# Kernel optimization log

Hardware: AMD Instinct MI355X
Metric: run time of the kernel (lower is better)

The kernel has to match this reference:

```python
import jax, jax.numpy as jnp
import numpy as np

N_NODES = 100000
N_EDGES = 1600000
C_IN = 128
C_OUT = 128


def setup_inputs() -> dict:
    key = jax.random.key(0)
    k1, k2, k3, k4, k5 = jax.random.split(key, 5)
    x = jax.random.normal(k1, (N_NODES, C_IN), dtype=jnp.float32)
    W = jax.random.normal(k2, (2 * C_IN, C_OUT), dtype=jnp.float32) * (1.0 / np.sqrt(2 * C_IN))
    b = jax.random.normal(k3, (C_OUT,), dtype=jnp.float32) * 0.01
    src = jax.random.randint(k4, (N_EDGES,), 0, N_NODES, dtype=jnp.int64 if jax.config.jax_enable_x64 else jnp.int32)
    dst = jax.random.randint(k5, (N_EDGES,), 0, N_NODES, dtype=jnp.int64 if jax.config.jax_enable_x64 else jnp.int32)
    return {"x": x, "W": W, "b": b, "src": src, "dst": dst}


def reference(x, W, b, src, dst):
    # Max-Relative graph conv: per-edge relative feature, max-aggregated per dst node.
    diff = x[dst] - x[src]                                  # [E, C]  (edge messages)
    max_diff = jax.ops.segment_max(diff, dst, num_segments=x.shape[0])  # [N, C]
    # Nodes with no incoming edges: segment_max yields -inf; zero them out.
    max_diff = jnp.where(jnp.isneginf(max_diff), jnp.zeros_like(max_diff), max_diff)
    h = jnp.concatenate([x, max_diff], axis=1)              # [N, 2C]
    return jax.nn.relu(h @ W + b)                           # Linear(2C->C_out) + ReLU
```

## Files before the change

### kernel.cpp

```cpp
#include <hip/hip_runtime.h>
#include <math.h>

#define NN 100000
#define NE 1600000
#define C 128

#define TS 4096
#define NT ((NE + TS - 1) / TS)
#define BUK ((NN + 511) >> 9)
#define NSC (BUK * NT)
#define NBS ((NSC + 2047) / 2048)
#define PREP_BLKS (NN * C / 8 / 256)
#define CONVW_BLKS (2 * C * C / 256)
#define GM 64

typedef __attribute__((ext_vector_type(8))) short          bf16x8;
typedef __attribute__((ext_vector_type(4))) float          f32x4;
typedef __attribute__((ext_vector_type(8))) unsigned short u16x8;
typedef unsigned short ushort_t;
typedef unsigned int   uint_t;

__device__ inline ushort_t f2bf(float f) {
    union { float f; uint_t u; } a; a.f = f;
    uint_t r = a.u + 0x7fff + ((a.u >> 16) & 1);
    return (ushort_t)(r >> 16);
}

__global__ __launch_bounds__(256) void k_setup(
        const float* __restrict__ x, ushort_t* __restrict__ xh,
        ushort_t* __restrict__ xt,
        const float* __restrict__ W, ushort_t* __restrict__ Wt,
        const int* __restrict__ dst, int* __restrict__ tileHistT) {
    __shared__ int h[BUK];
    const int t  = threadIdx.x;
    const int bb = blockIdx.x;
    if (bb < PREP_BLKS) {
        int i = bb * 256 + t;
        int node = i >> 4;
        int c0   = (i & 15) * 8;
        const float4* xp = (const float4*)(x + (long)i * 8);
        float4 v0 = xp[0], v1 = xp[1];
        ushort_t o[8] = { f2bf(v0.x), f2bf(v0.y), f2bf(v0.z), f2bf(v0.w),
                          f2bf(v1.x), f2bf(v1.y), f2bf(v1.z), f2bf(v1.w) };
        ushort_t tt[8];
        #pragma unroll
        for (int j = 0; j < 8; ++j)
            tt[j] = (o[j] & 0x8000) ? (ushort_t)~o[j] : (ushort_t)(o[j] | 0x8000);
        *(bf16x8*)(xh + (long)node * 256 + c0) = *(bf16x8*)o;
        *(bf16x8*)(xt + (long)node * 128 + c0) = *(bf16x8*)tt;
    } else if (bb < PREP_BLKS + CONVW_BLKS) {
        int i = (bb - PREP_BLKS) * 256 + t;
        int k = i >> 7, n = i & 127;
        Wt[n * 256 + k] = f2bf(W[i]);
    } else {
        const int tile = bb - PREP_BLKS - CONVW_BLKS;
        for (int i = t; i < BUK; i += 256) h[i] = 0;
        __syncthreads();
        const int base = tile * TS;
        for (int i = t; i < TS; i += 256) {
            int e = base + i;
            if (e < NE) atomicAdd(&h[dst[e] >> 9], 1);
        }
        __syncthreads();
        for (int i = t; i < BUK; i += 256) tileHistT[i * NT + tile] = h[i];
    }
}

__global__ __launch_bounds__(256) void scan_partial(const int* __restrict__ in,
                                                    int* __restrict__ out,
                                                    int* __restrict__ blocksums,
                                                    int n) {
    __shared__ int ts[256];
    const int t = threadIdx.x;
    const int base = blockIdx.x * 2048 + t * 8;
    int c[8];
    int s = 0;
    #pragma unroll
    for (int j = 0; j < 8; ++j) {
        int i = base + j;
        c[j] = (i < n) ? in[i] : 0;
        s += c[j];
    }
    ts[t] = s;
    __syncthreads();
    for (int off = 1; off < 256; off <<= 1) {
        int add = (t >= off) ? ts[t - off] : 0;
        __syncthreads();
        ts[t] += add;
        __syncthreads();
    }
    int run = (t == 0) ? 0 : ts[t - 1];
    #pragma unroll
    for (int j = 0; j < 8; ++j) {
        int i = base + j;
        if (i < n) out[i] = run;
        run += c[j];
    }
    if (t == 255) blocksums[blockIdx.x] = ts[255];
}

__device__ inline void scan_bsums_lds(const int* __restrict__ blocksums,
                                      int* bbase, int t) {
    if (t < 64) {
        int v = (t < NBS) ? blocksums[t] : 0;
        int incl = v;
        #pragma unroll
        for (int off = 1; off < 64; off <<= 1) {
            int nbr = __shfl_up(incl, off, 64);
            if (t >= off) incl += nbr;
        }
        bbase[t] = incl - v;
    }
}

__global__ __launch_bounds__(256) void p3_scatter(const int* __restrict__ dst,
                                                  const int* __restrict__ src,
                                                  const int* __restrict__ tileScan,
                                                  const int* __restrict__ blocksums,
                                                  uint_t* __restrict__ coarse) {
    __shared__ int cur[BUK];
    __shared__ int bbase[64];
    const int t = threadIdx.x, tile = blockIdx.x;
    scan_bsums_lds(blocksums, bbase, t);
    __syncthreads();
    for (int i = t; i < BUK; i += 256) {
        int idx = i * NT + tile;
        cur[i] = tileScan[idx] + bbase[idx >> 11];
    }
    __syncthreads();
    const int base = tile * TS;
    for (int i = t; i < TS; i += 256) {
        int e = base + i;
        if (e < NE) {
            int d = dst[e];
            int p = atomicAdd(&cur[d >> 9], 1);
            coarse[p] = ((uint_t)(d & 511) << 17) | (uint_t)src[e];
        }
    }
}

__global__ __launch_bounds__(256) void p4_build(const uint_t* __restrict__ coarse,
                                                const int* __restrict__ tileScan,
                                                const int* __restrict__ blocksums,
                                                int* __restrict__ offs,
                                                int* __restrict__ ssrc) {
    __shared__ int cnt[512];
    __shared__ int ts[256];
    __shared__ int bbase[64];
    const int b = blockIdx.x, t = threadIdx.x;
    scan_bsums_lds(blocksums, bbase, t);
    const int n0 = b << 9;
    cnt[t] = 0; cnt[t + 256] = 0;
    __syncthreads();
    const int i0 = b * NT;
    const int bs = tileScan[i0] + bbase[i0 >> 11];
    int be;
    if (b == BUK - 1) be = NE;
    else { int i1 = (b + 1) * NT; be = tileScan[i1] + bbase[i1 >> 11]; }
    for (int i = bs + t; i < be; i += 256)
        atomicAdd(&cnt[(int)(coarse[i] >> 17)], 1);
    __syncthreads();
    int c0 = cnt[2 * t], c1 = cnt[2 * t + 1];
    ts[t] = c0 + c1;
    __syncthreads();
    for (int off = 1; off < 256; off <<= 1) {
        int add = (t >= off) ? ts[t - off] : 0;
        __syncthreads();
        ts[t] += add;
        __syncthreads();
    }
    int ex = (t == 0) ? 0 : ts[t - 1];
    int o0 = bs + ex, o1 = o0 + c0;
    cnt[2 * t] = o0; cnt[2 * t + 1] = o1;
    if (n0 + 2 * t < NN)     offs[n0 + 2 * t]     = o0;
    if (n0 + 2 * t + 1 < NN) offs[n0 + 2 * t + 1] = o1;
    if (b == BUK - 1 && t == 0) offs[NN] = NE;
    __syncthreads();
    for (int i = bs + t; i < be; i += 256) {
        uint_t pk = coarse[i];
        int p = atomicAdd(&cnt[(int)(pk >> 17)], 1);
        ssrc[p] = (int)(pk & 0x1FFFF);
    }
}

__global__ __launch_bounds__(256) void node_min_v3(
        const int* __restrict__ offs, const int* __restrict__ ssrc,
        const ushort_t* __restrict__ xt, ushort_t* __restrict__ xh) {
    const int wid  = (blockIdx.x * 256 + threadIdx.x) >> 6;
    const int lane = threadIdx.x & 63;
    if (wid >= NN) return;
    const int g = lane >> 4;
    const int s = lane & 15;
    const int beg = offs[wid], end = offs[wid + 1];
    const char* xb = (const char*)xt;
    u16x8 vm;
    #pragma unroll
    for (int j = 0; j < 8; ++j) vm[j] = 0xFFFFu;
    int i = beg;
    for (; i + 8 <= end; i += 8) {
        int e0 = ssrc[i + g];
        int e1 = ssrc[i + 4 + g];
        u16x8 a = *(const u16x8*)(xb + (long)e0 * 256 + s * 16);
        u16x8 bq = *(const u16x8*)(xb + (long)e1 * 256 + s * 16);
        vm = __builtin_elementwise_min(vm, a);
        vm = __builtin_elementwise_min(vm, bq);
    }
    for (; i < end; i += 4) {
        int e = i + g;
        int idx = ssrc[(e < end) ? e : (end - 1)];
        u16x8 a = *(const u16x8*)(xb + (long)idx * 256 + s * 16);
        if (e < end) vm = __builtin_elementwise_min(vm, a);
    }
    union { u16x8 v; uint_t u[4]; } cv, ov;
    cv.v = vm;
    #pragma unroll
    for (int j = 0; j < 4; ++j) ov.u[j] = __shfl_xor(cv.u[j], 16, 64);
    cv.v = __builtin_elementwise_min(cv.v, ov.v);
    #pragma unroll
    for (int j = 0; j < 4; ++j) ov.u[j] = __shfl_xor(cv.u[j], 32, 64);
    cv.v = __builtin_elementwise_min(cv.v, ov.v);

    if (g == 0) {
        const bool has = end > beg;
        uint4 xd = *(const uint4*)((const char*)xh + (long)wid * 512 + s * 16);
        uint_t xu[4] = { xd.x, xd.y, xd.z, xd.w };
        uint4 o;
        uint_t* op = (uint_t*)&o;
        #pragma unroll
        for (int j = 0; j < 4; ++j) {
            ushort_t t0 = cv.v[2 * j], t1 = cv.v[2 * j + 1];
            ushort_t b0 = (t0 & 0x8000) ? (ushort_t)(t0 ^ 0x8000) : (ushort_t)~t0;
            ushort_t b1 = (t1 & 0x8000) ? (ushort_t)(t1 ^ 0x8000) : (ushort_t)~t1;
            float lo = has ? (__uint_as_float(xu[j] << 16)
                              - __uint_as_float((uint_t)b0 << 16)) : 0.0f;
            float hi = has ? (__uint_as_float(xu[j] & 0xffff0000u)
                              - __uint_as_float((uint_t)b1 << 16)) : 0.0f;
            op[j] = (uint_t)f2bf(lo) | ((uint_t)f2bf(hi) << 16);
        }
        *(uint4*)((char*)xh + (long)wid * 512 + 256 + s * 16) = o;
    }
}

__global__ __launch_bounds__(256) void gemm_mfma(
        const ushort_t* __restrict__ xh, const ushort_t* __restrict__ Wt,
        const float* __restrict__ b, float* __restrict__ out) {
    const int w    = threadIdx.x >> 6;
    const int l    = threadIdx.x & 63;
    const int wcol = w * 32;
    const int lr   = l & 15;
    const int kb   = (l >> 4) * 8;

    bf16x8 bb[2][8];
    float  bv[2];
    #pragma unroll
    for (int n = 0; n < 2; ++n) {
        int col = wcol + n * 16 + lr;
        bv[n] = b[col];
        const ushort_t* wp = Wt + (long)col * 256 + kb;
        #pragma unroll
        for (int k0 = 0; k0 < 8; ++k0)
            bb[n][k0] = *(const bf16x8*)(wp + k0 * 32);
    }

    const int mb0 = blockIdx.x * GM;
    #pragma unroll
    for (int mt = 0; mt < GM / 16; ++mt) {
        int mbase = mb0 + mt * 16;
        int arow = mbase + lr;
        if (arow >= NN) arow = NN - 1;
        const ushort_t* ap = xh + (long)arow * 256 + kb;
        bf16x8 a[8];
        #pragma unroll
        for (int k0 = 0; k0 < 8; ++k0) a[k0] = *(const bf16x8*)(ap + k0 * 32);

        f32x4 acc0 = (f32x4){0.f, 0.f, 0.f, 0.f};
        f32x4 acc1 = (f32x4){0.f, 0.f, 0.f, 0.f};
        #pragma unroll
        for (int k0 = 0; k0 < 8; ++k0) {
            acc0 = __builtin_amdgcn_mfma_f32_16x16x32_bf16(a[k0], bb[0][k0], acc0, 0, 0, 0);
            acc1 = __builtin_amdgcn_mfma_f32_16x16x32_bf16(a[k0], bb[1][k0], acc1, 0, 0, 0);
        }

        int rbase = mbase + ((l >> 4) << 2);
        int col0 = wcol + lr;
        #pragma unroll
        for (int j = 0; j < 4; ++j) {
            int r = rbase + j;
            if (r < NN) {
                out[(long)r * 128 + col0]      = fmaxf(acc0[j] + bv[0], 0.0f);
                out[(long)r * 128 + col0 + 16] = fmaxf(acc1[j] + bv[1], 0.0f);
            }
        }
    }
}

__global__ void init_neginf(float* __restrict__ p, int n) {
    int i = blockIdx.x * blockDim.x + threadIdx.x;
    if (i < n) p[i] = -INFINITY;
}

__device__ inline void amaxf(float* a, float v, float cur) {
    if (cur >= v) return;
    if (v >= 0.0f) atomicMax((int*)a, __float_as_int(v));
    else           atomicMin((unsigned int*)a, __float_as_uint(v));
}

__global__ __launch_bounds__(256) void edge_max(
        const float* __restrict__ x, const int* __restrict__ src,
        const int* __restrict__ dst, float* __restrict__ maxdiff) {
    long tid = (long)blockIdx.x * blockDim.x + threadIdx.x;
    int e = (int)(tid >> 5);
    if (e >= NE) return;
    int lane = (int)(tid & 31);
    int s = src[e], d = dst[e];
    int c0 = lane * 4;
    const float4 xd = *(const float4*)(x + (long)d * C + c0);
    const float4 xs = *(const float4*)(x + (long)s * C + c0);
    float4 df;
    df.x = xd.x - xs.x; df.y = xd.y - xs.y;
    df.z = xd.z - xs.z; df.w = xd.w - xs.w;
    float* o = maxdiff + (long)d * C + c0;
    float4 cur = *(const float4*)o;
    amaxf(o + 0, df.x, cur.x);
    amaxf(o + 1, df.y, cur.y);
    amaxf(o + 2, df.z, cur.z);
    amaxf(o + 3, df.w, cur.w);
}

#define TN 32
__global__ __launch_bounds__(256) void gemm_relu(
        const float* __restrict__ x, const float* __restrict__ W,
        const float* __restrict__ b, float* __restrict__ out) {
    __shared__ float h[TN][2 * C];
    const int nb = blockIdx.x * TN;
    const int t  = threadIdx.x;
    for (int i = t; i < TN * 2 * C / 4; i += 256) {
        int idx  = i * 4;
        int node = idx / (2 * C);
        int ci   = idx % (2 * C);
        float4 v;
        if (ci < C) {
            v = *(const float4*)(x + (long)(nb + node) * C + ci);
        } else {
            v = *(const float4*)(out + (long)(nb + node) * C + (ci - C));
            if (v.x == -INFINITY) v.x = 0.0f;
            if (v.y == -INFINITY) v.y = 0.0f;
            if (v.z == -INFINITY) v.z = 0.0f;
            if (v.w == -INFINITY) v.w = 0.0f;
        }
        *(float4*)&h[node][ci] = v;
    }
    __syncthreads();
    const int co = (t & 31) * 4;
    const int n0 = (t >> 5) * 4;
    float acc[4][4];
    #pragma unroll
    for (int i = 0; i < 4; ++i)
        #pragma unroll
        for (int j = 0; j < 4; ++j) acc[i][j] = 0.0f;
    for (int ci = 0; ci < 2 * C; ++ci) {
        float4 w = *(const float4*)(W + (long)ci * C + co);
        #pragma unroll
        for (int i = 0; i < 4; ++i) {
            float hv = h[n0 + i][ci];
            acc[i][0] = fmaf(hv, w.x, acc[i][0]);
            acc[i][1] = fmaf(hv, w.y, acc[i][1]);
            acc[i][2] = fmaf(hv, w.z, acc[i][2]);
            acc[i][3] = fmaf(hv, w.w, acc[i][3]);
        }
    }
    float4 bias = *(const float4*)(b + co);
    #pragma unroll
    for (int i = 0; i < 4; ++i) {
        float4 r;
        r.x = fmaxf(acc[i][0] + bias.x, 0.0f);
        r.y = fmaxf(acc[i][1] + bias.y, 0.0f);
        r.z = fmaxf(acc[i][2] + bias.z, 0.0f);
        r.w = fmaxf(acc[i][3] + bias.w, 0.0f);
        *(float4*)(out + (long)(nb + n0 + i) * C + co) = r;
    }
}

extern "C" void kernel_launch(void* const* d_in, const int* in_sizes, int n_in,
                              void* d_out, int out_size, void* d_ws, size_t ws_size,
                              hipStream_t stream) {
    const float* x   = (const float*)d_in[0];
    const float* W   = (const float*)d_in[1];
    const float* b   = (const float*)d_in[2];
    const int*   src = (const int*)d_in[3];
    const int*   dst = (const int*)d_in[4];
    float* out = (float*)d_out;

    size_t ints_head = (size_t)128 + NSC + (NN + 1) + NE;
    size_t head_b    = ((ints_head * 4) + 255) & ~(size_t)255;
    size_t xh_b      = (size_t)NN * 256 * 2;
    size_t wt_b      = (size_t)2 * C * C * 2;
    size_t need      = head_b + xh_b + wt_b;

    if (ws_size >= need) {
        int* blocksums = (int*)d_ws;
        int* tileScan  = blocksums + 128;
        int* offs      = tileScan + NSC;
        int* ssrc      = offs + NN + 1;
        ushort_t* xh   = (ushort_t*)((char*)d_ws + head_b);
        ushort_t* Wt   = (ushort_t*)((char*)d_ws + head_b + xh_b);
        int*      tileHistT = ssrc;
        uint_t*   coarse    = (uint_t*)d_out;
        ushort_t* xt        = (ushort_t*)((char*)d_out + (8u << 20));

        k_setup<<<PREP_BLKS + CONVW_BLKS + NT, 256, 0, stream>>>(x, xh, xt, W, Wt, dst, tileHistT);
        scan_partial<<<NBS, 256, 0, stream>>>(tileHistT, tileScan, blocksums, NSC);
        p3_scatter<<<NT, 256, 0, stream>>>(dst, src, tileScan, blocksums, coarse);
        p4_build<<<BUK, 256, 0, stream>>>(coarse, tileScan, blocksums, offs, ssrc);
        node_min_v3<<<NN / 4, 256, 0, stream>>>(offs, ssrc, xt, xh);
        gemm_mfma<<<(NN + GM - 1) / GM, 256, 0, stream>>>(xh, Wt, b, out);
    } else {
        int n = NN * C;
        init_neginf<<<(n + 255) / 256, 256, 0, stream>>>(out, n);
        long threads = (long)NE * 32;
        edge_max<<<(int)((threads + 255) / 256), 256, 0, stream>>>(x, src, dst, out);
        gemm_relu<<<(NN + TN - 1) / TN, 256, 0, stream>>>(x, W, b, out);
    }
}
```

Baseline: 272.0 us.

## Split node min-gather across channel slices with packed 32-bit lanes

Measured after the change: 557.0 us. 105% more time.

```diff
diff --git a/kernel.cpp b/kernel.cpp
--- a/kernel.cpp
+++ b/kernel.cpp
@@ -16,7 +16,7 @@
 
 typedef __attribute__((ext_vector_type(8))) short          bf16x8;
 typedef __attribute__((ext_vector_type(4))) float          f32x4;
-typedef __attribute__((ext_vector_type(8))) unsigned short u16x8;
+typedef __attribute__((ext_vector_type(2))) unsigned short u16x2;
 typedef unsigned short ushort_t;
 typedef unsigned int   uint_t;
 
@@ -24,6 +24,13 @@
     union { float f; uint_t u; } a; a.f = f;
     uint_t r = a.u + 0x7fff + ((a.u >> 16) & 1);
     return (ushort_t)(r >> 16);
+}
+
+__device__ inline uint_t pkmin(uint_t a, uint_t b) {
+    union { uint_t u; u16x2 v; } x, y, r;
+    x.u = a; y.u = b;
+    r.v = __builtin_elementwise_min(x.v, y.v);
+    return r.u;
 }
 
 __global__ __launch_bounds__(256) void k_setup(
@@ -183,61 +190,52 @@
     }
 }
 
-__global__ __launch_bounds__(256) void node_min_v3(
+__global__ __launch_bounds__(256) void node_min_v4(
         const int* __restrict__ offs, const int* __restrict__ ssrc,
         const ushort_t* __restrict__ xt, ushort_t* __restrict__ xh) {
-    const int wid  = (blockIdx.x * 256 + threadIdx.x) >> 6;
-    const int lane = threadIdx.x & 63;
+    const int slice = blockIdx.x & 7;
+    const int wid   = (blockIdx.x >> 3) * 4 + (threadIdx.x >> 6);
+    const int lane  = threadIdx.x & 63;
     if (wid >= NN) return;
-    const int g = lane >> 4;
-    const int s = lane & 15;
+    const int g = lane >> 3;
+    const int c = lane & 7;
     const int beg = offs[wid], end = offs[wid + 1];
-    const char* xb = (const char*)xt;
-    u16x8 vm;
-    #pragma unroll
-    for (int j = 0; j < 8; ++j) vm[j] = 0xFFFFu;
+    const uint_t* xp = (const uint_t*)xt + slice * 8 + c;
+
+    uint_t vm = 0xFFFFFFFFu;
     int i = beg;
-    for (; i + 8 <= end; i += 8) {
-        int e0 = ssrc[i + g];
-        int e1 = ssrc[i + 4 + g];
-        u16x8 a = *(const u16x8*)(xb + (long)e0 * 256 + s * 16);
-        u16x8 bq = *(const u16x8*)(xb + (long)e1 * 256 + s * 16);
-        vm = __builtin_elementwise_min(vm, a);
-        vm = __builtin_elementwise_min(vm, bq);
-    }
-    for (; i < end; i += 4) {
+    for (; i + 16 <= end; i += 16) {
+        int e0 = __builtin_nontemporal_load(&ssrc[i + g]);
+        int e1 = __builtin_nontemporal_load(&ssrc[i + 8 + g]);
+        uint_t a  = xp[(long)e0 * 64];
+        uint_t bq = xp[(long)e1 * 64];
+        vm = pkmin(vm, a);
+        vm = pkmin(vm, bq);
+    }
+    for (; i < end; i += 8) {
         int e = i + g;
-        int idx = ssrc[(e < end) ? e : (end - 1)];
-        u16x8 a = *(const u16x8*)(xb + (long)idx * 256 + s * 16);
-        if (e < end) vm = __builtin_elementwise_min(vm, a);
-    }
-    union { u16x8 v; uint_t u[4]; } cv, ov;
-    cv.v = vm;
-    #pragma unroll
-    for (int j = 0; j < 4; ++j) ov.u[j] = __shfl_xor(cv.u[j], 16, 64);
-    cv.v = __builtin_elementwise_min(cv.v, ov.v);
-    #pragma unroll
-    for (int j = 0; j < 4; ++j) ov.u[j] = __shfl_xor(cv.u[j], 32, 64);
-    cv.v = __builtin_elementwise_min(cv.v, ov.v);
+        int idx = __builtin_nontemporal_load(&ssrc[(e < end) ? e : (end - 1)]);
+        uint_t a = xp[(long)idx * 64];
+        if (e < end) vm = pkmin(vm, a);
+    }
+    vm = pkmin(vm, __shfl_xor(vm, 8, 64));
+    vm = pkmin(vm, __shfl_xor(vm, 16, 64));
+    vm = pkmin(vm, __shfl_xor(vm, 32, 64));
 
     if (g == 0) {
         const bool has = end > beg;
-        uint4 xd = *(const uint4*)((const char*)xh + (long)wid * 512 + s * 16);
-        uint_t xu[4] = { xd.x, xd.y, xd.z, xd.w };
-        uint4 o;
-        uint_t* op = (uint_t*)&o;
-        #pragma unroll
-        for (int j = 0; j < 4; ++j) {
-            ushort_t t0 = cv.v[2 * j], t1 = cv.v[2 * j + 1];
-            ushort_t b0 = (t0 & 0x8000) ? (ushort_t)(t0 ^ 0x8000) : (ushort_t)~t0;
-            ushort_t b1 = (t1 & 0x8000) ? (ushort_t)(t1 ^ 0x8000) : (ushort_t)~t1;
-            float lo = has ? (__uint_as_float(xu[j] << 16)
-                              - __uint_as_float((uint_t)b0 << 16)) : 0.0f;
-            float hi = has ? (__uint_as_float(xu[j] & 0xffff0000u)
-                              - __uint_as_float((uint_t)b1 << 16)) : 0.0f;
-            op[j] = (uint_t)f2bf(lo) | ((uint_t)f2bf(hi) << 16);
-        }
-        *(uint4*)((char*)xh + (long)wid * 512 + 256 + s * 16) = o;
+        const uint_t* xr = (const uint_t*)xh + (long)wid * 128 + slice * 8 + c;
+        uint_t xu = __builtin_nontemporal_load(xr);
+        ushort_t t0 = (ushort_t)(vm & 0xFFFF), t1 = (ushort_t)(vm >> 16);
+        ushort_t b0 = (t0 & 0x8000) ? (ushort_t)(t0 ^ 0x8000) : (ushort_t)~t0;
+        ushort_t b1 = (t1 & 0x8000) ? (ushort_t)(t1 ^ 0x8000) : (ushort_t)~t1;
+        float lo = has ? (__uint_as_float(xu << 16)
+                          - __uint_as_float((uint_t)b0 << 16)) : 0.0f;
+        float hi = has ? (__uint_as_float(xu & 0xffff0000u)
+                          - __uint_as_float((uint_t)b1 << 16)) : 0.0f;
+        uint_t o = (uint_t)f2bf(lo) | ((uint_t)f2bf(hi) << 16);
+        uint_t* ow = (uint_t*)xh + (long)wid * 128 + 64 + slice * 8 + c;
+        __builtin_nontemporal_store(o, ow);
     }
 }
 
@@ -412,7 +410,7 @@
         scan_partial<<<NBS, 256, 0, stream>>>(tileHistT, tileScan, blocksums, NSC);
         p3_scatter<<<NT, 256, 0, stream>>>(dst, src, tileScan, blocksums, coarse);
         p4_build<<<BUK, 256, 0, stream>>>(coarse, tileScan, blocksums, offs, ssrc);
-        node_min_v3<<<NN / 4, 256, 0, stream>>>(offs, ssrc, xt, xh);
+        node_min_v4<<<(NN / 4) * 8, 256, 0, stream>>>(offs, ssrc, xt, xh);
         gemm_mfma<<<(NN + GM - 1) / GM, 256, 0, stream>>>(xh, Wt, b, out);
     } else {
         int n = NN * C;
```
